# Kernel tuning notes

Measured on AMD Instinct MI355X. Metric: run time of the kernel, lower is better.

## Reference

```python
import jax, jax.numpy as jnp
import numpy as np

NH, NOPE_D, ROPE_D, V_D, R = 16, 48, 16, 64, 128
EPS = 1e-6

def rms_norm(x, w):
    norm = jax.lax.rsqrt(jnp.mean(jnp.square(x), axis=-1, keepdims=True) + EPS)
    return x * norm * w

def apply_rope(x, cos, sin):
    # x: (..., rope_d); cos/sin broadcastable (..., rope_d//2)
    d = x.shape[-1]
    x1, x2 = x[..., : d // 2], x[..., d // 2 :]
    return jnp.concatenate([x1 * cos - x2 * sin, x2 * cos + x1 * sin], axis=-1)

def setup_inputs() -> dict:
    key = jax.random.key(0)
    ks = jax.random.split(key, 8)
    B, T, D = 2, 2048, 1024
    s = lambda fan_in: 1.0 / np.sqrt(fan_in)
    return {
        "x": jax.random.normal(ks[0], (B, T, D), jnp.float32),
        "cos": jax.random.uniform(ks[1], (T, ROPE_D // 2), jnp.float32),
        "sin": jax.random.uniform(ks[2], (T, ROPE_D // 2), jnp.float32),
        "Wq": jax.random.normal(ks[3], (NH * (NOPE_D + ROPE_D), D), jnp.float32) * s(D),
        "q_norm_w": jnp.ones((NOPE_D + ROPE_D,), jnp.float32),
        "Wkva": jax.random.normal(ks[4], (R + ROPE_D, D), jnp.float32) * s(D),
        "kva_norm_w": jnp.ones((R,), jnp.float32),
        "Wkvb": jax.random.normal(ks[5], (NH * (NOPE_D + V_D), R), jnp.float32) * s(R),
        "Wo": jax.random.normal(ks[6], (D, NH * V_D), jnp.float32) * s(NH * V_D),
    }

def reference(x, cos, sin, Wq, q_norm_w, Wkva, kva_norm_w, Wkvb, Wo):
    B, T, D = x.shape
    # Q path: project, per-head RMSNorm over (nope+rope) dims, split
    q = (x @ Wq.T).reshape(B, T, NH, NOPE_D + ROPE_D)
    q = rms_norm(q, q_norm_w)
    q_nope, q_rope = q[..., :NOPE_D], q[..., NOPE_D:]
    # Low-rank KV path
    kv_a = x @ Wkva.T  # (B,T,R+ROPE_D)
    kv_latent = rms_norm(kv_a[..., :R], kva_norm_w)
    k_rope_raw = kv_a[..., R:]  # (B,T,ROPE_D) shared across heads
    kv_b = (kv_latent @ Wkvb.T).reshape(B, T, NH, NOPE_D + V_D)
    k_nope, v = kv_b[..., :NOPE_D], kv_b[..., NOPE_D:]
    # Decoupled RoPE
    cos_t = cos[None, :T, None, :]  # (1,T,1,rope_d/2)
    sin_t = sin[None, :T, None, :]
    q_rope = apply_rope(q_rope, cos_t, sin_t)
    k_rope = apply_rope(k_rope_raw[:, :, None, :], cos[None, :T, None, :], sin[None, :T, None, :])
    k_rope = jnp.broadcast_to(k_rope, (B, T, NH, ROPE_D))
    q_full = jnp.concatenate([q_nope, q_rope], axis=-1)  # (B,T,NH,64)
    k_full = jnp.concatenate([k_nope, k_rope], axis=-1)
    # Causal attention, scale = 1/sqrt(nope+rope)
    scale = (NOPE_D + ROPE_D) ** -0.5
    scores = jnp.einsum("bqhd,bkhd->bhqk", q_full, k_full) * scale
    causal = jnp.tril(jnp.ones((T, T), bool))
    scores = jnp.where(causal[None, None], scores, -jnp.inf)
    attn = jax.nn.softmax(scores, axis=-1)
    out = jnp.einsum("bhqk,bkhd->bqhd", attn, v).reshape(B, T, NH * V_D)
    return out @ Wo.T
```

## Files before the change

### kernel.cpp

```cpp
#include <hip/hip_runtime.h>
#include <hip/hip_bf16.h>
#include <math.h>

#define NH 16
#define T_ 2048
#define B_ 2
#define D_ 1024
#define EPS 1e-6f

typedef __attribute__((ext_vector_type(8))) short bf16x8;
typedef __attribute__((ext_vector_type(4))) short bf16x4;
typedef __attribute__((ext_vector_type(4))) float f32x4;

__device__ __forceinline__ float wred_sum(float v){
  #pragma unroll
  for (int o = 32; o > 0; o >>= 1) v += __shfl_xor(v, o, 64);
  return v;
}

__device__ __forceinline__ unsigned pack_bf16(float a, float b){
  __hip_bfloat162 t = __float22bfloat162_rn(make_float2(a, b));
  unsigned r; __builtin_memcpy(&r, &t, 4); return r;
}

__device__ __forceinline__ void gload_lds16(const void* g, void* l){
  __builtin_amdgcn_global_load_lds((const __attribute__((address_space(1))) void*)g,
                                   (__attribute__((address_space(3))) void*)l, 16, 0, 0);
}

__device__ __forceinline__ f32x4 mfma16(bf16x4 a, bf16x4 b, f32x4 c){
#if __has_builtin(__builtin_amdgcn_mfma_f32_16x16x16bf16_1k)
  return __builtin_amdgcn_mfma_f32_16x16x16bf16_1k(a, b, c, 0, 0, 0);
#else
  asm volatile("v_mfma_f32_16x16x16_bf16 %0, %1, %2, %0" : "+v"(c) : "v"(a), "v"(b));
  return c;
#endif
}

__global__ __launch_bounds__(256)
void cvt5(const float* __restrict__ x, const float* __restrict__ wq,
          const float* __restrict__ wkva, const float* __restrict__ wkvb,
          const float* __restrict__ wo,
          __hip_bfloat16* __restrict__ xb, __hip_bfloat16* __restrict__ wqb,
          __hip_bfloat16* __restrict__ wkvab, __hip_bfloat16* __restrict__ wkvbb,
          __hip_bfloat16* __restrict__ wob)
{
  const int i = blockIdx.x * 256 + threadIdx.x;
  const float* s; __hip_bfloat16* d; size_t soff, doff;
  if      (i < 1048576) { s = x;    d = xb;    soff = doff = i; }
  else if (i < 1310720) { s = wq;   d = wqb;   soff = doff = i - 1048576; }
  else if (i < 1347584) { s = wkva; d = wkvab; soff = doff = i - 1310720; }
  else if (i < 1404928) {
    const int off = i - 1347584;
    const int srow = off >> 5, c4 = off & 31;
    const int h = srow / 112, dd = srow % 112;
    const int drow = (dd < 48) ? (h*48 + dd) : (768 + h*64 + (dd - 48));
    s = wkvb; d = wkvbb; soff = off; doff = (size_t)drow*32 + c4;
  }
  else                  { s = wo;   d = wob;   soff = doff = i - 1404928; }
  float4 v = *(const float4*)(s + soff * 4);
  *(__hip_bfloat162*)(d + doff * 4)     = __float22bfloat162_rn(make_float2(v.x, v.y));
  *(__hip_bfloat162*)(d + doff * 4 + 2) = __float22bfloat162_rn(make_float2(v.z, v.w));
}

template<typename CT>
__global__ __launch_bounds__(256, 2)
void gemm_bt64(const __hip_bfloat16* __restrict__ A, const __hip_bfloat16* __restrict__ W,
               CT* __restrict__ C, int M, int N, int K)
{
  __shared__ __hip_bfloat16 As[2][128 * 64];
  __shared__ __hip_bfloat16 Ws[2][64 * 64];
  const int tid = threadIdx.x;
  const int wv = tid >> 6, lane = tid & 63;
  const int m = lane & 15, quad = lane >> 4;
  const int bm = blockIdx.y * 128, bn = blockIdx.x * 64;

  const __hip_bfloat16* ga[4];
  const __hip_bfloat16* gw[2];
  #pragma unroll
  for (int i = 0; i < 4; i++) {
    const int slot = i*256 + tid;
    const int row = slot >> 3, cb = slot & 7;
    ga[i] = A + (size_t)(bm + row) * K + ((cb ^ (row & 7)) << 3);
  }
  #pragma unroll
  for (int i = 0; i < 2; i++) {
    const int slot = i*256 + tid;
    const int row = slot >> 3, cb = slot & 7;
    int wr = bn + row; if (wr >= N) wr = N - 1;
    gw[i] = W + (size_t)wr * K + ((cb ^ (row & 7)) << 3);
  }
  auto stage = [&](int buf){
    #pragma unroll
    for (int i = 0; i < 4; i++) { gload_lds16(ga[i], &As[buf][(i*256 + wv*64)*8]); ga[i] += 64; }
    #pragma unroll
    for (int i = 0; i < 2; i++) { gload_lds16(gw[i], &Ws[buf][(i*256 + wv*64)*8]); gw[i] += 64; }
  };

  f32x4 acc[2][4];
  #pragma unroll
  for (int mi = 0; mi < 2; mi++)
    #pragma unroll
    for (int nj = 0; nj < 4; nj++) acc[mi][nj] = (f32x4){0.f,0.f,0.f,0.f};

  stage(0);
  const int iters = K >> 6;
  for (int it = 0; it < iters; it++) {
    const int cur = it & 1;
    __syncthreads();
    if (it + 1 < iters) stage(cur ^ 1);
    #pragma unroll
    for (int ks = 0; ks < 2; ks++) {
      const int cb = ((ks*4 + quad) ^ (m & 7)) << 3;
      bf16x8 af[2], wf[4];
      #pragma unroll
      for (int mi = 0; mi < 2; mi++)
        af[mi] = *(const bf16x8*)(&As[cur][(wv*32 + mi*16 + m) * 64 + cb]);
      #pragma unroll
      for (int nj = 0; nj < 4; nj++)
        wf[nj] = *(const bf16x8*)(&Ws[cur][(nj*16 + m) * 64 + cb]);
      #pragma unroll
      for (int mi = 0; mi < 2; mi++)
        #pragma unroll
        for (int nj = 0; nj < 4; nj++)
          acc[mi][nj] = __builtin_amdgcn_mfma_f32_16x16x32_bf16(af[mi], wf[nj], acc[mi][nj], 0, 0, 0);
    }
  }

  #pragma unroll
  for (int mi = 0; mi < 2; mi++)
    #pragma unroll
    for (int nj = 0; nj < 4; nj++) {
      const int col = bn + nj*16 + m;
      if (col < N) {
        #pragma unroll
        for (int r = 0; r < 4; r++) {
          const int row = bm + wv*32 + mi*16 + quad*4 + r;
          if constexpr (sizeof(CT) == 2)
            C[(size_t)row * N + col] = (CT)__float2bfloat16(acc[mi][nj][r]);
          else
            C[(size_t)row * N + col] = acc[mi][nj][r];
        }
      }
    }
}

__global__ __launch_bounds__(256, 2)
void gemm_qkva(const __hip_bfloat16* __restrict__ A, const __hip_bfloat16* __restrict__ Wqb,
               const __hip_bfloat16* __restrict__ Wkvab,
               const float* __restrict__ qw, const float* __restrict__ cosp,
               const float* __restrict__ sinp,
               __hip_bfloat16* __restrict__ qb, float* __restrict__ kva)
{
  __shared__ __hip_bfloat16 As[2][128 * 64];
  __shared__ __hip_bfloat16 Ws[2][64 * 64];
  const int K = 1024;
  const int tid = threadIdx.x;
  const int wv = tid >> 6, lane = tid & 63;
  const int m = lane & 15, quad = lane >> 4;
  const int bm = blockIdx.y * 128;
  const bool isq = blockIdx.x < 16;
  const __hip_bfloat16* W = isq ? Wqb : Wkvab;
  const int bn = isq ? blockIdx.x*64 : (blockIdx.x - 16)*64;
  const int Nw = isq ? 1024 : 144;

  const __hip_bfloat16* ga[4];
  const __hip_bfloat16* gw[2];
  #pragma unroll
  for (int i = 0; i < 4; i++) {
    const int slot = i*256 + tid;
    const int row = slot >> 3, cb = slot & 7;
    ga[i] = A + (size_t)(bm + row) * K + ((cb ^ (row & 7)) << 3);
  }
  #pragma unroll
  for (int i = 0; i < 2; i++) {
    const int slot = i*256 + tid;
    const int row = slot >> 3, cb = slot & 7;
    int wr = bn + row; if (wr >= Nw) wr = Nw - 1;
    gw[i] = W + (size_t)wr * K + ((cb ^ (row & 7)) << 3);
  }
  auto stage = [&](int buf){
    #pragma unroll
    for (int i = 0; i < 4; i++) { gload_lds16(ga[i], &As[buf][(i*256 + wv*64)*8]); ga[i] += 64; }
    #pragma unroll
    for (int i = 0; i < 2; i++) { gload_lds16(gw[i], &Ws[buf][(i*256 + wv*64)*8]); gw[i] += 64; }
  };

  f32x4 acc[2][4];
  #pragma unroll
  for (int mi = 0; mi < 2; mi++)
    #pragma unroll
    for (int nj = 0; nj < 4; nj++) acc[mi][nj] = (f32x4){0.f,0.f,0.f,0.f};

  stage(0);
  for (int it = 0; it < 16; it++) {
    const int cur = it & 1;
    __syncthreads();
    if (it < 15) stage(cur ^ 1);
    #pragma unroll
    for (int ks = 0; ks < 2; ks++) {
      const int cb = ((ks*4 + quad) ^ (m & 7)) << 3;
      bf16x8 af[2], wf[4];
      #pragma unroll
      for (int mi = 0; mi < 2; mi++)
        af[mi] = *(const bf16x8*)(&As[cur][(wv*32 + mi*16 + m) * 64 + cb]);
      #pragma unroll
      for (int nj = 0; nj < 4; nj++)
        wf[nj] = *(const bf16x8*)(&Ws[cur][(nj*16 + m) * 64 + cb]);
      #pragma unroll
      for (int mi = 0; mi < 2; mi++)
        #pragma unroll
        for (int nj = 0; nj < 4; nj++)
          acc[mi][nj] = __builtin_amdgcn_mfma_f32_16x16x32_bf16(af[mi], wf[nj], acc[mi][nj], 0, 0, 0);
    }
  }

  if (isq) {
    const int head = blockIdx.x;
    float qwv[4];
    #pragma unroll
    for (int nj = 0; nj < 4; nj++) qwv[nj] = qw[nj*16 + m];
    const int j = m & 7;
    const float qscale = 0.125f * 1.44269504f;
    #pragma unroll
    for (int mi = 0; mi < 2; mi++) {
      #pragma unroll
      for (int r = 0; r < 4; r++) {
        float ss = 0.f;
        #pragma unroll
        for (int nj = 0; nj < 4; nj++) { const float t = acc[mi][nj][r]; ss = fmaf(t, t, ss); }
        ss += __shfl_xor(ss, 1, 64); ss += __shfl_xor(ss, 2, 64);
        ss += __shfl_xor(ss, 4, 64); ss += __shfl_xor(ss, 8, 64);
        const float nrm = rsqrtf(ss * (1.0f/64.0f) + EPS);
        float v[4];
        #pragma unroll
        for (int nj = 0; nj < 4; nj++) v[nj] = acc[mi][nj][r] * nrm * qwv[nj];
        const int grow = bm + wv*32 + mi*16 + quad*4 + r;
        const int t = grow & (T_ - 1);
        const int b = grow >> 11;
        const float part = __shfl_xor(v[3], 8, 64);
        const float c = cosp[t*8 + j], sn = sinp[t*8 + j];
        v[3] = (m < 8) ? (v[3]*c - part*sn) : (v[3]*c + part*sn);
        __hip_bfloat16* dst = qb + ((size_t)(b*NH + head)*T_ + t)*64 + m;
        #pragma unroll
        for (int nj = 0; nj < 4; nj++) dst[nj*16] = __float2bfloat16(v[nj] * qscale);
      }
    }
  } else {
    #pragma unroll
    for (int mi = 0; mi < 2; mi++)
      #pragma unroll
      for (int nj = 0; nj < 4; nj++) {
        const int col = bn + nj*16 + m;
        if (col < 144) {
          #pragma unroll
          for (int r = 0; r < 4; r++) {
            const int row = bm + wv*32 + mi*16 + quad*4 + r;
            kva[(size_t)row * 144 + col] = acc[mi][nj][r];
          }
        }
      }
  }
}

__global__ void prep_kv(const float* __restrict__ kva, const float* __restrict__ kw,
                        const float* __restrict__ cosp, const float* __restrict__ sinp,
                        __hip_bfloat16* __restrict__ kvl16, __hip_bfloat16* __restrict__ krope16)
{
  const int tid = threadIdx.x;
  const int bt = blockIdx.x;
  const int t = bt % T_;
  const float* row = kva + (size_t)bt * 144;
  const float v = row[tid];
  float s = wred_sum(v * v);
  __shared__ float red[2];
  if ((tid & 63) == 0) red[tid >> 6] = s;
  __syncthreads();
  const float total = red[0] + red[1];
  const float norm = rsqrtf(total * (1.0f/128.0f) + EPS);
  kvl16[(size_t)bt * 128 + tid] = __float2bfloat16(v * norm * kw[tid]);
  if (tid < 16) {
    const int j = tid & 7;
    const float c = cosp[t*8 + j], sn = sinp[t*8 + j];
    const float x1 = row[128 + j], x2 = row[136 + j];
    krope16[(size_t)bt * 16 + tid] = __float2bfloat16((tid < 8) ? (x1 * c - x2 * sn)
                                                               : (x2 * c + x1 * sn));
  }
}

__global__ __launch_bounds__(256, 2)
void gemm_kvb(const __hip_bfloat16* __restrict__ A, const __hip_bfloat16* __restrict__ W,
              __hip_bfloat16* __restrict__ knope, __hip_bfloat16* __restrict__ vt)
{
  __shared__ __hip_bfloat16 As[2][128 * 64];
  __shared__ __hip_bfloat16 Ws[2][64 * 64];
  const int K = 128;
  const int tid = threadIdx.x;
  const int wv = tid >> 6, lane = tid & 63;
  const int m = lane & 15, quad = lane >> 4;
  const int bm = blockIdx.y * 128, bn = blockIdx.x * 64;

  const __hip_bfloat16* ga[4];
  const __hip_bfloat16* gw[2];
  #pragma unroll
  for (int i = 0; i < 4; i++) {
    const int slot = i*256 + tid;
    const int row = slot >> 3, cb = slot & 7;
    ga[i] = A + (size_t)(bm + row) * K + ((cb ^ (row & 7)) << 3);
  }
  #pragma unroll
  for (int i = 0; i < 2; i++) {
    const int slot = i*256 + tid;
    const int row = slot >> 3, cb = slot & 7;
    gw[i] = W + (size_t)(bn + row) * K + ((cb ^ (row & 7)) << 3);
  }
  auto stage = [&](int buf){
    #pragma unroll
    for (int i = 0; i < 4; i++) { gload_lds16(ga[i], &As[buf][(i*256 + wv*64)*8]); ga[i] += 64; }
    #pragma unroll
    for (int i = 0; i < 2; i++) { gload_lds16(gw[i], &Ws[buf][(i*256 + wv*64)*8]); gw[i] += 64; }
  };

  f32x4 acc[2][4];
  #pragma unroll
  for (int mi = 0; mi < 2; mi++)
    #pragma unroll
    for (int nj = 0; nj < 4; nj++) acc[mi][nj] = (f32x4){0.f,0.f,0.f,0.f};

  stage(0);
  for (int it = 0; it < 2; it++) {
    const int cur = it & 1;
    __syncthreads();
    if (it == 0) stage(1);
    #pragma unroll
    for (int ks = 0; ks < 2; ks++) {
      const int cb = ((ks*4 + quad) ^ (m & 7)) << 3;
      bf16x8 af[2], wf[4];
      #pragma unroll
      for (int mi = 0; mi < 2; mi++)
        af[mi] = *(const bf16x8*)(&As[cur][(wv*32 + mi*16 + m) * 64 + cb]);
      #pragma unroll
      for (int nj = 0; nj < 4; nj++)
        wf[nj] = *(const bf16x8*)(&Ws[cur][(nj*16 + m) * 64 + cb]);
      #pragma unroll
      for (int mi = 0; mi < 2; mi++)
        #pragma unroll
        for (int nj = 0; nj < 4; nj++)
          acc[mi][nj] = __builtin_amdgcn_mfma_f32_16x16x32_bf16(af[mi], wf[nj], acc[mi][nj], 0, 0, 0);
    }
  }

  if (bn < 768) {
    #pragma unroll
    for (int mi = 0; mi < 2; mi++)
      #pragma unroll
      for (int nj = 0; nj < 4; nj++) {
        const int col = bn + nj*16 + m;
        #pragma unroll
        for (int r = 0; r < 4; r++) {
          const int row = bm + wv*32 + mi*16 + quad*4 + r;
          knope[(size_t)row * 768 + col] = __float2bfloat16(acc[mi][nj][r]);
        }
      }
  } else {
    __syncthreads();
    short* TL = (short*)&As[0][0];
    #pragma unroll
    for (int mi = 0; mi < 2; mi++)
      #pragma unroll
      for (int nj = 0; nj < 4; nj++) {
        const int d = nj*16 + m;
        #pragma unroll
        for (int r = 0; r < 4; r++) {
          const int tl = wv*32 + mi*16 + quad*4 + r;
          __hip_bfloat16 hv = __float2bfloat16(acc[mi][nj][r]);
          short sv; __builtin_memcpy(&sv, &hv, 2);
          TL[d*136 + tl] = sv;
        }
      }
    __syncthreads();
    const int h = (bn - 768) >> 6;
    const int b = bm >> 11;
    const int t0 = bm & (T_ - 1);
    #pragma unroll
    for (int i = 0; i < 4; i++) {
      const int unit = i*256 + tid;
      const int d = unit >> 4, tu = unit & 15;
      *(bf16x8*)(vt + ((size_t)(b*NH + h)*64 + d)*T_ + t0 + tu*8)
          = *(const bf16x8*)(TL + d*136 + tu*8);
    }
  }
}

__global__ __launch_bounds__(256, 4)
void attn_tile(const __hip_bfloat16* __restrict__ qb,
               const __hip_bfloat16* __restrict__ knope,
               const __hip_bfloat16* __restrict__ krope16,
               const __hip_bfloat16* __restrict__ vt16,
               __hip_bfloat16* __restrict__ aout)
{
  __shared__ __hip_bfloat16 SL[16384];
  const int tid = threadIdx.x;
  const int wv = tid >> 6, lane = tid & 63;
  const int m = lane & 15, quad = lane >> 4;
  const int wq = wv >> 1, wk = wv & 1;
  const int idx = (blockIdx.x + blockIdx.y) & 31;
  const int pj = idx & 7, pk = idx >> 3;
  const int qt = (pk == 0) ? pj : (pk == 1) ? (15 - pj) : (pk == 2) ? (16 + pj) : (31 - pj);
  const int bh = blockIdx.y;
  const int b = bh >> 4, h = bh & 15;
  const int nt = qt + 1;

  bf16x8 q0[2], q1[2];
  #pragma unroll
  for (int t2 = 0; t2 < 2; t2++) {
    const __hip_bfloat16* qr = qb + ((size_t)bh*T_ + qt*64 + wq*32 + t2*16 + m)*64 + quad*8;
    q0[t2] = *(const bf16x8*)qr; q1[t2] = *(const bf16x8*)(qr + 32);
  }

  const __hip_bfloat16* pK[2]; size_t iK[2];
  const __hip_bfloat16* pV[2];
  #pragma unroll
  for (int i = 0; i < 2; i++) {
    const int slot = i*256 + tid;
    const int krow = slot >> 3;
    const int kde = (slot & 7) ^ (krow & 7);
    if (kde < 6) { pK[i] = knope + (size_t)(b*T_ + krow)*768 + h*48 + kde*8; iK[i] = (size_t)64*768; }
    else         { pK[i] = krope16 + (size_t)(b*T_ + krow)*16 + (kde-6)*8;   iK[i] = (size_t)64*16; }
    pV[i] = vt16 + ((size_t)bh*64 + krow)*T_ + kde*8;
  }

  auto stage = [&](int buf){
    #pragma unroll
    for (int i = 0; i < 2; i++) {
      gload_lds16(pK[i], SL + buf*4096 + (i*256 + wv*64)*8);
      gload_lds16(pV[i], SL + 8192 + buf*4096 + (i*256 + wv*64)*8);
      pK[i] += iK[i]; pV[i] += 64;
    }
  };

  f32x4 o[2][4];
  #pragma unroll
  for (int t2 = 0; t2 < 2; t2++)
    #pragma unroll
    for (int vs = 0; vs < 4; vs++) o[t2][vs] = (f32x4){0.f,0.f,0.f,0.f};
  float lrun[2] = {0.f, 0.f};

  const int swk = quad ^ (m & 7);
  const int qh = quad >> 1, ql = quad & 1;
  stage(0);

  for (int kt = 0; kt < nt; kt++) {
    const int cur = kt & 1;
    __syncthreads();
    if (kt + 1 < nt) stage(cur ^ 1);
    const __hip_bfloat16* Kc = SL + cur*4096;
    const __hip_bfloat16* Vc = SL + 8192 + cur*4096;
    const bool dtile = (kt == qt);

    f32x4 s[2][2];
    __builtin_amdgcn_s_setprio(1);
    #pragma unroll
    for (int ks = 0; ks < 2; ks++) {
      const int gk2 = 2*wk + ks;
      if (!dtile || gk2 <= 2*wq + 1) {
        const __hip_bfloat16* kr = Kc + (wk*32 + ks*16 + m)*64;
        const bf16x8 kf0 = *(const bf16x8*)(kr + swk*8);
        const bf16x8 kf1 = *(const bf16x8*)(kr + (swk^4)*8);
        #pragma unroll
        for (int t2 = 0; t2 < 2; t2++) {
          if (!dtile || gk2 <= 2*wq + t2) {
            f32x4 z = (f32x4){0.f,0.f,0.f,0.f};
            z = __builtin_amdgcn_mfma_f32_16x16x32_bf16(kf0, q0[t2], z, 0, 0, 0);
            z = __builtin_amdgcn_mfma_f32_16x16x32_bf16(kf1, q1[t2], z, 0, 0, 0);
            s[t2][ks] = z;
          } else {
            s[t2][ks] = (f32x4){-1e30f,-1e30f,-1e30f,-1e30f};
          }
        }
      } else {
        s[0][ks] = (f32x4){-1e30f,-1e30f,-1e30f,-1e30f};
        s[1][ks] = (f32x4){-1e30f,-1e30f,-1e30f,-1e30f};
      }
    }
    __builtin_amdgcn_s_setprio(0);

    if (dtile) {
      #pragma unroll
      for (int ks = 0; ks < 2; ks++)
        #pragma unroll
        for (int t2 = 0; t2 < 2; t2++)
          if (2*wk + ks == 2*wq + t2) {
            #pragma unroll
            for (int r = 0; r < 4; r++)
              if (quad*4 + r > m) s[t2][ks][r] = -1e30f;
          }
    }

    bf16x4 u[2][2];
    #pragma unroll
    for (int t2 = 0; t2 < 2; t2++)
      #pragma unroll
      for (int ks = 0; ks < 2; ks++) {
        float p0 = exp2f(s[t2][ks][0] - 48.0f), p1 = exp2f(s[t2][ks][1] - 48.0f);
        float p2 = exp2f(s[t2][ks][2] - 48.0f), p3 = exp2f(s[t2][ks][3] - 48.0f);
        lrun[t2] += (p0 + p1) + (p2 + p3);
        union { unsigned ui[2]; bf16x4 v; } uu;
        uu.ui[0] = pack_bf16(p0, p1);
        uu.ui[1] = pack_bf16(p2, p3);
        u[t2][ks] = uu.v;
      }

    __builtin_amdgcn_s_setprio(1);
    #pragma unroll
    for (int vs = 0; vs < 4; vs++) {
      #pragma unroll
      for (int ks = 0; ks < 2; ks++) {
        const int gk2 = 2*wk + ks;
        if (!dtile || gk2 <= 2*wq + 1) {
          const bf16x4 vf = *(const bf16x4*)(Vc + (vs*16 + m)*64
                              + (((wk*4 + ks*2 + qh) ^ (m & 7)) << 3) + (ql << 2));
          #pragma unroll
          for (int t2 = 0; t2 < 2; t2++)
            if (!dtile || gk2 <= 2*wq + t2)
              o[t2][vs] = mfma16(vf, u[t2][ks], o[t2][vs]);
        }
      }
    }
    __builtin_amdgcn_s_setprio(0);
  }

  __syncthreads();
  float* FB = (float*)SL;
  float* LB = ((float*)SL) + 4096;
  if (wk == 1) {
    #pragma unroll
    for (int t2 = 0; t2 < 2; t2++)
      #pragma unroll
      for (int vs = 0; vs < 4; vs++)
        #pragma unroll
        for (int r = 0; r < 4; r++)
          FB[wq*2048 + ((t2*4 + vs)*4 + r)*64 + lane] = o[t2][vs][r];
    LB[wq*128 + lane]      = lrun[0];
    LB[wq*128 + 64 + lane] = lrun[1];
  }
  __syncthreads();
  if (wk == 0) {
    #pragma unroll
    for (int t2 = 0; t2 < 2; t2++)
      #pragma unroll
      for (int vs = 0; vs < 4; vs++)
        #pragma unroll
        for (int r = 0; r < 4; r++)
          o[t2][vs][r] += FB[wq*2048 + ((t2*4 + vs)*4 + r)*64 + lane];
    lrun[0] += LB[wq*128 + lane];
    lrun[1] += LB[wq*128 + 64 + lane];
    #pragma unroll
    for (int t2 = 0; t2 < 2; t2++) {
      float l = lrun[t2];
      l += __shfl_xor(l, 16, 64);
      l += __shfl_xor(l, 32, 64);
      const float inv = 1.0f / l;
      const size_t base = (size_t)(b*T_ + qt*64 + wq*32 + t2*16 + m) * 1024 + h*64 + quad*4;
      #pragma unroll
      for (int vs = 0; vs < 4; vs++) {
        union { unsigned ui[2]; bf16x4 v; } pkv;
        pkv.ui[0] = pack_bf16(o[t2][vs][0] * inv, o[t2][vs][1] * inv);
        pkv.ui[1] = pack_bf16(o[t2][vs][2] * inv, o[t2][vs][3] * inv);
        *(bf16x4*)(aout + base + vs*16) = pkv.v;
      }
    }
  }
}

extern "C" void kernel_launch(void* const* d_in, const int* in_sizes, int n_in,
                              void* d_out, int out_size, void* d_ws, size_t ws_size,
                              hipStream_t stream)
{
  const float* x    = (const float*)d_in[0];
  const float* cosp = (const float*)d_in[1];
  const float* sinp = (const float*)d_in[2];
  const float* Wq   = (const float*)d_in[3];
  const float* qw   = (const float*)d_in[4];
  const float* Wkva = (const float*)d_in[5];
  const float* kw   = (const float*)d_in[6];
  const float* Wkvb = (const float*)d_in[7];
  const float* Wo   = (const float*)d_in[8];
  float* out = (float*)d_out;

  float* kva = (float*)d_ws;
  __hip_bfloat16* xb16    = (__hip_bfloat16*)(kva + 589824);
  __hip_bfloat16* knope16 = xb16 + 4194304;
  __hip_bfloat16* kvl16   = knope16 + 3145728;
  __hip_bfloat16* qb16    = kvl16 + 524288;
  __hip_bfloat16* vt16    = qb16 + 4194304;
  __hip_bfloat16* krope16 = vt16 + 4194304;
  __hip_bfloat16* Wqb     = krope16 + 65536;
  __hip_bfloat16* Wkvab   = Wqb + 1048576;
  __hip_bfloat16* Wkvbb   = Wkvab + 147456;
  __hip_bfloat16* Wob     = Wkvbb + 229376;
  __hip_bfloat16* ab16    = Wob + 1048576;

  const int M = B_ * T_;

  cvt5<<<6512, 256, 0, stream>>>(x, Wq, Wkva, Wkvb, Wo, xb16, Wqb, Wkvab, Wkvbb, Wob);
  gemm_qkva<<<dim3(19, 32), 256, 0, stream>>>(xb16, Wqb, Wkvab, qw, cosp, sinp, qb16, kva);
  prep_kv<<<M, 128, 0, stream>>>(kva, kw, cosp, sinp, kvl16, krope16);
  gemm_kvb<<<dim3(28, 32), 256, 0, stream>>>(kvl16, Wkvbb, knope16, vt16);
  attn_tile<<<dim3(32, B_ * NH), 256, 0, stream>>>(qb16, knope16, krope16, vt16, ab16);
  gemm_bt64<float><<<dim3(16, 32), 256, 0, stream>>>(ab16, Wob, out, M, 1024, 1024);
}
```

Measured before the change: 177.0 us.

## Fuse KV-latent RMSNorm and k-rope into QKVA GEMM with 128x128 tiles

```diff
diff --git a/kernel.cpp b/kernel.cpp
--- a/kernel.cpp
+++ b/kernel.cpp
@@ -11,12 +11,6 @@
 typedef __attribute__((ext_vector_type(8))) short bf16x8;
 typedef __attribute__((ext_vector_type(4))) short bf16x4;
 typedef __attribute__((ext_vector_type(4))) float f32x4;
-
-__device__ __forceinline__ float wred_sum(float v){
-  #pragma unroll
-  for (int o = 32; o > 0; o >>= 1) v += __shfl_xor(v, o, 64);
-  return v;
-}
 
 __device__ __forceinline__ unsigned pack_bf16(float a, float b){
   __hip_bfloat162 t = __float22bfloat162_rn(make_float2(a, b));
@@ -148,47 +142,44 @@
 __global__ __launch_bounds__(256, 2)
 void gemm_qkva(const __hip_bfloat16* __restrict__ A, const __hip_bfloat16* __restrict__ Wqb,
                const __hip_bfloat16* __restrict__ Wkvab,
-               const float* __restrict__ qw, const float* __restrict__ cosp,
-               const float* __restrict__ sinp,
-               __hip_bfloat16* __restrict__ qb, float* __restrict__ kva)
+               const float* __restrict__ qw, const float* __restrict__ kw,
+               const float* __restrict__ cosp, const float* __restrict__ sinp,
+               __hip_bfloat16* __restrict__ qb, __hip_bfloat16* __restrict__ kvl16,
+               __hip_bfloat16* __restrict__ krope16)
 {
   __shared__ __hip_bfloat16 As[2][128 * 64];
-  __shared__ __hip_bfloat16 Ws[2][64 * 64];
+  __shared__ __hip_bfloat16 Ws[2][128 * 64];
   const int K = 1024;
   const int tid = threadIdx.x;
   const int wv = tid >> 6, lane = tid & 63;
   const int m = lane & 15, quad = lane >> 4;
+  const int wr = wv >> 1, wc = wv & 1;
   const int bm = blockIdx.y * 128;
-  const bool isq = blockIdx.x < 16;
+  const bool isq = blockIdx.x < 8;
   const __hip_bfloat16* W = isq ? Wqb : Wkvab;
-  const int bn = isq ? blockIdx.x*64 : (blockIdx.x - 16)*64;
+  const int bn = isq ? blockIdx.x*128 : (blockIdx.x - 8)*128;
   const int Nw = isq ? 1024 : 144;
 
   const __hip_bfloat16* ga[4];
-  const __hip_bfloat16* gw[2];
+  const __hip_bfloat16* gw[4];
   #pragma unroll
   for (int i = 0; i < 4; i++) {
     const int slot = i*256 + tid;
     const int row = slot >> 3, cb = slot & 7;
     ga[i] = A + (size_t)(bm + row) * K + ((cb ^ (row & 7)) << 3);
-  }
-  #pragma unroll
-  for (int i = 0; i < 2; i++) {
-    const int slot = i*256 + tid;
-    const int row = slot >> 3, cb = slot & 7;
-    int wr = bn + row; if (wr >= Nw) wr = Nw - 1;
-    gw[i] = W + (size_t)wr * K + ((cb ^ (row & 7)) << 3);
+    int wrow = bn + row; if (wrow >= Nw) wrow = Nw - 1;
+    gw[i] = W + (size_t)wrow * K + ((cb ^ (row & 7)) << 3);
   }
   auto stage = [&](int buf){
     #pragma unroll
     for (int i = 0; i < 4; i++) { gload_lds16(ga[i], &As[buf][(i*256 + wv*64)*8]); ga[i] += 64; }
     #pragma unroll
-    for (int i = 0; i < 2; i++) { gload_lds16(gw[i], &Ws[buf][(i*256 + wv*64)*8]); gw[i] += 64; }
+    for (int i = 0; i < 4; i++) { gload_lds16(gw[i], &Ws[buf][(i*256 + wv*64)*8]); gw[i] += 64; }
   };
 
-  f32x4 acc[2][4];
-  #pragma unroll
-  for (int mi = 0; mi < 2; mi++)
+  f32x4 acc[4][4];
+  #pragma unroll
+  for (int mi = 0; mi < 4; mi++)
     #pragma unroll
     for (int nj = 0; nj < 4; nj++) acc[mi][nj] = (f32x4){0.f,0.f,0.f,0.f};
 
@@ -200,15 +191,15 @@
     #pragma unroll
     for (int ks = 0; ks < 2; ks++) {
       const int cb = ((ks*4 + quad) ^ (m & 7)) << 3;
-      bf16x8 af[2], wf[4];
-      #pragma unroll
-      for (int mi = 0; mi < 2; mi++)
-        af[mi] = *(const bf16x8*)(&As[cur][(wv*32 + mi*16 + m) * 64 + cb]);
+      bf16x8 af[4], wf[4];
+      #pragma unroll
+      for (int mi = 0; mi < 4; mi++)
+        af[mi] = *(const bf16x8*)(&As[cur][(wr*64 + mi*16 + m) * 64 + cb]);
       #pragma unroll
       for (int nj = 0; nj < 4; nj++)
-        wf[nj] = *(const bf16x8*)(&Ws[cur][(nj*16 + m) * 64 + cb]);
-      #pragma unroll
-      for (int mi = 0; mi < 2; mi++)
+        wf[nj] = *(const bf16x8*)(&Ws[cur][(wc*64 + nj*16 + m) * 64 + cb]);
+      #pragma unroll
+      for (int mi = 0; mi < 4; mi++)
         #pragma unroll
         for (int nj = 0; nj < 4; nj++)
           acc[mi][nj] = __builtin_amdgcn_mfma_f32_16x16x32_bf16(af[mi], wf[nj], acc[mi][nj], 0, 0, 0);
@@ -216,14 +207,14 @@
   }
 
   if (isq) {
-    const int head = blockIdx.x;
+    const int head = blockIdx.x*2 + wc;
     float qwv[4];
     #pragma unroll
     for (int nj = 0; nj < 4; nj++) qwv[nj] = qw[nj*16 + m];
     const int j = m & 7;
     const float qscale = 0.125f * 1.44269504f;
     #pragma unroll
-    for (int mi = 0; mi < 2; mi++) {
+    for (int mi = 0; mi < 4; mi++) {
       #pragma unroll
       for (int r = 0; r < 4; r++) {
         float ss = 0.f;
@@ -235,7 +226,7 @@
         float v[4];
         #pragma unroll
         for (int nj = 0; nj < 4; nj++) v[nj] = acc[mi][nj][r] * nrm * qwv[nj];
-        const int grow = bm + wv*32 + mi*16 + quad*4 + r;
+        const int grow = bm + wr*64 + mi*16 + quad*4 + r;
         const int t = grow & (T_ - 1);
         const int b = grow >> 11;
         const float part = __shfl_xor(v[3], 8, 64);
@@ -246,45 +237,54 @@
         for (int nj = 0; nj < 4; nj++) dst[nj*16] = __float2bfloat16(v[nj] * qscale);
       }
     }
+  } else if (bn == 0) {
+    __syncthreads();
+    float* P = (float*)As;
+    float part[4][4];
+    #pragma unroll
+    for (int mi = 0; mi < 4; mi++)
+      #pragma unroll
+      for (int r = 0; r < 4; r++) {
+        float ss = 0.f;
+        #pragma unroll
+        for (int nj = 0; nj < 4; nj++) { const float t = acc[mi][nj][r]; ss = fmaf(t, t, ss); }
+        ss += __shfl_xor(ss, 1, 64); ss += __shfl_xor(ss, 2, 64);
+        ss += __shfl_xor(ss, 4, 64); ss += __shfl_xor(ss, 8, 64);
+        part[mi][r] = ss;
+        if (m == 0) P[((wc*2 + wr)*4 + mi)*16 + quad*4 + r] = ss;
+      }
+    __syncthreads();
+    float kwv[4];
+    #pragma unroll
+    for (int nj = 0; nj < 4; nj++) kwv[nj] = kw[wc*64 + nj*16 + m];
+    #pragma unroll
+    for (int mi = 0; mi < 4; mi++)
+      #pragma unroll
+      for (int r = 0; r < 4; r++) {
+        const float tot = part[mi][r] + P[(((wc^1)*2 + wr)*4 + mi)*16 + quad*4 + r];
+        const float nrm = rsqrtf(tot * (1.0f/128.0f) + EPS);
+        const int row = bm + wr*64 + mi*16 + quad*4 + r;
+        #pragma unroll
+        for (int nj = 0; nj < 4; nj++)
+          kvl16[(size_t)row*128 + wc*64 + nj*16 + m]
+              = __float2bfloat16(acc[mi][nj][r] * nrm * kwv[nj]);
+      }
   } else {
-    #pragma unroll
-    for (int mi = 0; mi < 2; mi++)
-      #pragma unroll
-      for (int nj = 0; nj < 4; nj++) {
-        const int col = bn + nj*16 + m;
-        if (col < 144) {
-          #pragma unroll
-          for (int r = 0; r < 4; r++) {
-            const int row = bm + wv*32 + mi*16 + quad*4 + r;
-            kva[(size_t)row * 144 + col] = acc[mi][nj][r];
-          }
+    if (wc == 0) {
+      const int j = m & 7;
+      #pragma unroll
+      for (int mi = 0; mi < 4; mi++)
+        #pragma unroll
+        for (int r = 0; r < 4; r++) {
+          const int row = bm + wr*64 + mi*16 + quad*4 + r;
+          const int t = row & (T_ - 1);
+          const float v = acc[mi][0][r];
+          const float part = __shfl_xor(v, 8, 64);
+          const float c = cosp[t*8 + j], sn = sinp[t*8 + j];
+          krope16[(size_t)row*16 + m] = __float2bfloat16((m < 8) ? (v*c - part*sn)
+                                                                 : (v*c + part*sn));
         }
-      }
-  }
-}
-
-__global__ void prep_kv(const float* __restrict__ kva, const float* __restrict__ kw,
-                        const float* __restrict__ cosp, const float* __restrict__ sinp,
-                        __hip_bfloat16* __restrict__ kvl16, __hip_bfloat16* __restrict__ krope16)
-{
-  const int tid = threadIdx.x;
-  const int bt = blockIdx.x;
-  const int t = bt % T_;
-  const float* row = kva + (size_t)bt * 144;
-  const float v = row[tid];
-  float s = wred_sum(v * v);
-  __shared__ float red[2];
-  if ((tid & 63) == 0) red[tid >> 6] = s;
-  __syncthreads();
-  const float total = red[0] + red[1];
-  const float norm = rsqrtf(total * (1.0f/128.0f) + EPS);
-  kvl16[(size_t)bt * 128 + tid] = __float2bfloat16(v * norm * kw[tid]);
-  if (tid < 16) {
-    const int j = tid & 7;
-    const float c = cosp[t*8 + j], sn = sinp[t*8 + j];
-    const float x1 = row[128 + j], x2 = row[136 + j];
-    krope16[(size_t)bt * 16 + tid] = __float2bfloat16((tid < 8) ? (x1 * c - x2 * sn)
-                                                               : (x2 * c + x1 * sn));
+    }
   }
 }
 
@@ -604,8 +604,8 @@
   const int M = B_ * T_;
 
   cvt5<<<6512, 256, 0, stream>>>(x, Wq, Wkva, Wkvb, Wo, xb16, Wqb, Wkvab, Wkvbb, Wob);
-  gemm_qkva<<<dim3(19, 32), 256, 0, stream>>>(xb16, Wqb, Wkvab, qw, cosp, sinp, qb16, kva);
-  prep_kv<<<M, 128, 0, stream>>>(kva, kw, cosp, sinp, kvl16, krope16);
+  gemm_qkva<<<dim3(10, 32), 256, 0, stream>>>(xb16, Wqb, Wkvab, qw, kw, cosp, sinp,
+                                              qb16, kvl16, krope16);
   gemm_kvb<<<dim3(28, 32), 256, 0, stream>>>(kvl16, Wkvbb, knope16, vt16);
   attn_tile<<<dim3(32, B_ * NH), 256, 0, stream>>>(qb16, knope16, krope16, vt16, ab16);
   gemm_bt64<float><<<dim3(16, 32), 256, 0, stream>>>(ab16, Wob, out, M, 1024, 1024);
```

After: 178.0 us. Within noise of the previous version (+0.6%).
